# Optimization experiments

Hardware: AMD Instinct MI355X
Metric: run time of the kernel (lower is better)

Reference implementation:

```python
import jax, jax.numpy as jnp
import numpy as np

L = 2048
NODE_DIM = 64
EDGE_DIM = 32

def setup_inputs() -> dict:
    key = jax.random.key(0)
    ks = jax.random.split(key, 5)
    coords = jax.random.normal(ks[0], (L, 3), dtype=jnp.float32) * 10.0
    node_features = jax.random.normal(ks[1], (L, NODE_DIM), dtype=jnp.float32)
    pair_features = jax.random.normal(ks[2], (L, L, EDGE_DIM), dtype=jnp.float32)
    # haiku Linear params: w (in, out), b (out,)
    w_attn = jax.random.normal(ks[3], (EDGE_DIM + 1, 1), dtype=jnp.float32) / np.sqrt(EDGE_DIM + 1)
    b_attn = jnp.zeros((1,), dtype=jnp.float32)
    w_mag = jax.random.normal(ks[4], (NODE_DIM, 1), dtype=jnp.float32) / np.sqrt(NODE_DIM)
    b_mag = jnp.zeros((1,), dtype=jnp.float32)
    return {"coords": coords, "node_features": node_features, "pair_features": pair_features,
            "w_attn": w_attn, "b_attn": b_attn, "w_mag": w_mag, "b_mag": b_mag}

def reference(coords, node_features, pair_features, w_attn, b_attn, w_mag, b_mag):
    # displacements[i,j] = coords[i] - coords[j]  -> (L, L, 3)
    displacements = coords[:, None, :] - coords[None, :, :]
    distances = jnp.linalg.norm(displacements, axis=-1, keepdims=True) + 1e-08  # (L,L,1)
    directions = displacements / distances  # (L,L,3)
    # Linear(1) over concat(pair_features, distance): split the matvec to avoid concat copy
    # logits = [pair_features, dist] @ w_attn + b_attn  -> (L,L,1)
    attention_logits = (jnp.einsum('ije,eo->ijo', pair_features, w_attn[:-1])
                        + distances * w_attn[-1] + b_attn)
    attention_weights = jax.nn.softmax(attention_logits, axis=1)  # softmax over j-index axis 1
    update_magnitudes = jnp.tanh(node_features @ w_mag + b_mag) * 0.1  # (L,1)
    # sum over axis=1 of attn * dir * mag[:,None,:]
    coord_updates = jnp.sum(attention_weights * directions, axis=1) * update_magnitudes  # (L,3)
    return coords + coord_updates
```

## Files before the change

kernel.cpp:

```cpp
#include <hip/hip_runtime.h>
#include <math.h>

#define LL 2048
#define NODE_DIM 64
#define EDGE_DIM 32
#define LOG2E 1.4426950408889634f

typedef float vfloat4 __attribute__((ext_vector_type(4)));

__global__ __launch_bounds__(256, 6) void se3_layer_kernel(
    const float* __restrict__ coords,
    const float* __restrict__ node_features,
    const float* __restrict__ pair,
    const float* __restrict__ w_attn,
    const float* __restrict__ b_attn,
    const float* __restrict__ w_mag,
    const float* __restrict__ b_mag,
    float* __restrict__ out)
{
    __shared__ float s_cx[LL], s_cy[LL], s_cz[LL];
    __shared__ float s_mag;
    __shared__ float r_m[4], r_s[4], r_ax[4], r_ay[4], r_az[4];

    const int i    = blockIdx.x;
    const int tid  = threadIdx.x;
    const int lane = tid & 63;
    const int wave = tid >> 6;
    const int sub  = lane & 7;
    const int grp  = lane >> 3;

    for (int j = tid; j < LL; j += 256) {
        s_cx[j] = coords[3 * j + 0];
        s_cy[j] = coords[3 * j + 1];
        s_cz[j] = coords[3 * j + 2];
    }

    if (tid < NODE_DIM) {
        float v = node_features[(size_t)i * NODE_DIM + tid] * w_mag[tid];
        #pragma unroll
        for (int off = 32; off; off >>= 1) v += __shfl_xor(v, off);
        if (tid == 0) s_mag = tanhf(v + b_mag[0]) * 0.1f;
    }
    __syncthreads();

    const float w0 = w_attn[4 * sub + 0] * LOG2E;
    const float w1 = w_attn[4 * sub + 1] * LOG2E;
    const float w2 = w_attn[4 * sub + 2] * LOG2E;
    const float w3 = w_attn[4 * sub + 3] * LOG2E;
    const float wd = w_attn[EDGE_DIM] * LOG2E;
    const float bb = b_attn[0] * LOG2E;
    const float cix = s_cx[i], ciy = s_cy[i], ciz = s_cz[i];

    float m = -INFINITY, s = 0.f, ax = 0.f, ay = 0.f, az = 0.f;

    const vfloat4* prow = (const vfloat4*)(pair + (size_t)i * LL * EDGE_DIM);

    auto process = [&](vfloat4 v, int jbase) {
        float dotv = v.x * w0 + v.y * w1 + v.z * w2 + v.w * w3;
        dotv += __shfl_xor(dotv, 1);
        dotv += __shfl_xor(dotv, 2);
        dotv += __shfl_xor(dotv, 4);

        const int j = jbase + grp;
        float dx = cix - s_cx[j], dy = ciy - s_cy[j], dz = ciz - s_cz[j];
        float d2 = fmaf(dx, dx, fmaf(dy, dy, dz * dz));
        d2 = fmaxf(d2, 1e-24f);
        float r    = __builtin_amdgcn_rsqf(d2);
        float dist = d2 * r;
        float logit = fmaf(dist, wd, dotv + bb);

        float mn    = fmaxf(m, logit);
        float scale = __builtin_amdgcn_exp2f(m - mn);
        float pw    = __builtin_amdgcn_exp2f(logit - mn);
        s  = fmaf(s,  scale, pw);
        float px = pw * r;
        ax = fmaf(ax, scale, px * dx);
        ay = fmaf(ay, scale, px * dy);
        az = fmaf(az, scale, px * dz);
        m = mn;
    };

    int J = wave * 16;
    vfloat4 a0 = __builtin_nontemporal_load(&prow[(size_t)J * 8 + lane]);
    vfloat4 a1 = __builtin_nontemporal_load(&prow[(size_t)(J + 8) * 8 + lane]);
    for (int it = 1; it < 32; ++it) {
        const int Jn = it * 64 + wave * 16;
        vfloat4 b0 = __builtin_nontemporal_load(&prow[(size_t)Jn * 8 + lane]);
        vfloat4 b1 = __builtin_nontemporal_load(&prow[(size_t)(Jn + 8) * 8 + lane]);
        process(a0, J);
        process(a1, J + 8);
        a0 = b0; a1 = b1; J = Jn;
    }
    process(a0, J);
    process(a1, J + 8);

    #pragma unroll
    for (int off = 32; off; off >>= 1) {
        float m2  = __shfl_xor(m,  off);
        float s2  = __shfl_xor(s,  off);
        float ax2 = __shfl_xor(ax, off);
        float ay2 = __shfl_xor(ay, off);
        float az2 = __shfl_xor(az, off);
        float M  = fmaxf(m, m2);
        float c1 = __builtin_amdgcn_exp2f(m - M), c2 = __builtin_amdgcn_exp2f(m2 - M);
        s  = s  * c1 + s2  * c2;
        ax = ax * c1 + ax2 * c2;
        ay = ay * c1 + ay2 * c2;
        az = az * c1 + az2 * c2;
        m = M;
    }

    if (lane == 0) {
        r_m[wave] = m; r_s[wave] = s;
        r_ax[wave] = ax; r_ay[wave] = ay; r_az[wave] = az;
    }
    __syncthreads();

    if (tid == 0) {
        float M = r_m[0], S = r_s[0], AX = r_ax[0], AY = r_ay[0], AZ = r_az[0];
        #pragma unroll
        for (int w = 1; w < 4; ++w) {
            float M2 = r_m[w];
            float Mn = fmaxf(M, M2);
            float c1 = __builtin_amdgcn_exp2f(M - Mn), c2 = __builtin_amdgcn_exp2f(M2 - Mn);
            S  = S  * c1 + r_s[w]  * c2;
            AX = AX * c1 + r_ax[w] * c2;
            AY = AY * c1 + r_ay[w] * c2;
            AZ = AZ * c1 + r_az[w] * c2;
            M = Mn;
        }
        float inv_s = 1.0f / S;
        float mg = s_mag;
        out[3 * i + 0] = coords[3 * i + 0] + AX * inv_s * mg;
        out[3 * i + 1] = coords[3 * i + 1] + AY * inv_s * mg;
        out[3 * i + 2] = coords[3 * i + 2] + AZ * inv_s * mg;
    }
}

extern "C" void kernel_launch(void* const* d_in, const int* in_sizes, int n_in,
                              void* d_out, int out_size, void* d_ws, size_t ws_size,
                              hipStream_t stream) {
    const float* coords        = (const float*)d_in[0];
    const float* node_features = (const float*)d_in[1];
    const float* pair          = (const float*)d_in[2];
    const float* w_attn        = (const float*)d_in[3];
    const float* b_attn        = (const float*)d_in[4];
    const float* w_mag         = (const float*)d_in[5];
    const float* b_mag         = (const float*)d_in[6];
    float* out = (float*)d_out;

    se3_layer_kernel<<<LL, 256, 0, stream>>>(coords, node_features, pair,
                                             w_attn, b_attn, w_mag, b_mag, out);
}
```

Baseline: 92.58 us.

## Process two query rows per block to reuse coordinate tile and halve blocks

```diff
diff --git a/kernel.cpp b/kernel.cpp
--- a/kernel.cpp
+++ b/kernel.cpp
@@ -8,7 +8,7 @@
 
 typedef float vfloat4 __attribute__((ext_vector_type(4)));
 
-__global__ __launch_bounds__(256, 6) void se3_layer_kernel(
+__global__ __launch_bounds__(256, 4) void se3_layer_kernel(
     const float* __restrict__ coords,
     const float* __restrict__ node_features,
     const float* __restrict__ pair,
@@ -19,15 +19,23 @@
     float* __restrict__ out)
 {
     __shared__ float s_cx[LL], s_cy[LL], s_cz[LL];
-    __shared__ float s_mag;
-    __shared__ float r_m[4], r_s[4], r_ax[4], r_ay[4], r_az[4];
+    __shared__ float s_mag[2];
+    __shared__ float r_m[2][4], r_s[2][4], r_ax[2][4], r_ay[2][4], r_az[2][4];
 
-    const int i    = blockIdx.x;
+    const int i0   = 2 * blockIdx.x;
+    const int i1   = i0 + 1;
     const int tid  = threadIdx.x;
     const int lane = tid & 63;
     const int wave = tid >> 6;
     const int sub  = lane & 7;
     const int grp  = lane >> 3;
+
+    const vfloat4* prow0 = (const vfloat4*)(pair + (size_t)i0 * LL * EDGE_DIM);
+    const vfloat4* prow1 = (const vfloat4*)(pair + (size_t)i1 * LL * EDGE_DIM);
+
+    int J = wave * 8;
+    vfloat4 a0 = __builtin_nontemporal_load(&prow0[(size_t)J * 8 + lane]);
+    vfloat4 a1 = __builtin_nontemporal_load(&prow1[(size_t)J * 8 + lane]);
 
     for (int j = tid; j < LL; j += 256) {
         s_cx[j] = coords[3 * j + 0];
@@ -35,11 +43,11 @@
         s_cz[j] = coords[3 * j + 2];
     }
 
-    if (tid < NODE_DIM) {
-        float v = node_features[(size_t)i * NODE_DIM + tid] * w_mag[tid];
+    if (wave < 2) {
+        float v = node_features[(size_t)(i0 + wave) * NODE_DIM + lane] * w_mag[lane];
         #pragma unroll
         for (int off = 32; off; off >>= 1) v += __shfl_xor(v, off);
-        if (tid == 0) s_mag = tanhf(v + b_mag[0]) * 0.1f;
+        if (lane == 0) s_mag[wave] = tanhf(v + b_mag[0]) * 0.1f;
     }
     __syncthreads();
 
@@ -49,91 +57,113 @@
     const float w3 = w_attn[4 * sub + 3] * LOG2E;
     const float wd = w_attn[EDGE_DIM] * LOG2E;
     const float bb = b_attn[0] * LOG2E;
-    const float cix = s_cx[i], ciy = s_cy[i], ciz = s_cz[i];
+    const float c0x = s_cx[i0], c0y = s_cy[i0], c0z = s_cz[i0];
+    const float c1x = s_cx[i1], c1y = s_cy[i1], c1z = s_cz[i1];
 
-    float m = -INFINITY, s = 0.f, ax = 0.f, ay = 0.f, az = 0.f;
+    float m0 = -INFINITY, s0 = 0.f, ax0 = 0.f, ay0 = 0.f, az0 = 0.f;
+    float m1 = -INFINITY, s1 = 0.f, ax1 = 0.f, ay1 = 0.f, az1 = 0.f;
 
-    const vfloat4* prow = (const vfloat4*)(pair + (size_t)i * LL * EDGE_DIM);
-
-    auto process = [&](vfloat4 v, int jbase) {
-        float dotv = v.x * w0 + v.y * w1 + v.z * w2 + v.w * w3;
-        dotv += __shfl_xor(dotv, 1);
-        dotv += __shfl_xor(dotv, 2);
-        dotv += __shfl_xor(dotv, 4);
+    auto process = [&](vfloat4 v0, vfloat4 v1, int jbase) {
+        float d0 = v0.x * w0 + v0.y * w1 + v0.z * w2 + v0.w * w3;
+        float d1 = v1.x * w0 + v1.y * w1 + v1.z * w2 + v1.w * w3;
+        d0 += __shfl_xor(d0, 1);  d1 += __shfl_xor(d1, 1);
+        d0 += __shfl_xor(d0, 2);  d1 += __shfl_xor(d1, 2);
+        d0 += __shfl_xor(d0, 4);  d1 += __shfl_xor(d1, 4);
 
         const int j = jbase + grp;
-        float dx = cix - s_cx[j], dy = ciy - s_cy[j], dz = ciz - s_cz[j];
-        float d2 = fmaf(dx, dx, fmaf(dy, dy, dz * dz));
-        d2 = fmaxf(d2, 1e-24f);
-        float r    = __builtin_amdgcn_rsqf(d2);
-        float dist = d2 * r;
-        float logit = fmaf(dist, wd, dotv + bb);
+        const float cx = s_cx[j], cy = s_cy[j], cz = s_cz[j];
 
-        float mn    = fmaxf(m, logit);
-        float scale = __builtin_amdgcn_exp2f(m - mn);
-        float pw    = __builtin_amdgcn_exp2f(logit - mn);
-        s  = fmaf(s,  scale, pw);
-        float px = pw * r;
-        ax = fmaf(ax, scale, px * dx);
-        ay = fmaf(ay, scale, px * dy);
-        az = fmaf(az, scale, px * dz);
-        m = mn;
+        {
+            float dx = c0x - cx, dy = c0y - cy, dz = c0z - cz;
+            float d2 = fmaf(dx, dx, fmaf(dy, dy, dz * dz));
+            d2 = fmaxf(d2, 1e-24f);
+            float r    = __builtin_amdgcn_rsqf(d2);
+            float dist = d2 * r;
+            float logit = fmaf(dist, wd, d0 + bb);
+            float mn    = fmaxf(m0, logit);
+            float scale = __builtin_amdgcn_exp2f(m0 - mn);
+            float pw    = __builtin_amdgcn_exp2f(logit - mn);
+            s0  = fmaf(s0,  scale, pw);
+            float px = pw * r;
+            ax0 = fmaf(ax0, scale, px * dx);
+            ay0 = fmaf(ay0, scale, px * dy);
+            az0 = fmaf(az0, scale, px * dz);
+            m0 = mn;
+        }
+        {
+            float dx = c1x - cx, dy = c1y - cy, dz = c1z - cz;
+            float d2 = fmaf(dx, dx, fmaf(dy, dy, dz * dz));
+            d2 = fmaxf(d2, 1e-24f);
+            float r    = __builtin_amdgcn_rsqf(d2);
+            float dist = d2 * r;
+            float logit = fmaf(dist, wd, d1 + bb);
+            float mn    = fmaxf(m1, logit);
+            float scale = __builtin_amdgcn_exp2f(m1 - mn);
+            float pw    = __builtin_amdgcn_exp2f(logit - mn);
+            s1  = fmaf(s1,  scale, pw);
+            float px = pw * r;
+            ax1 = fmaf(ax1, scale, px * dx);
+            ay1 = fmaf(ay1, scale, px * dy);
+            az1 = fmaf(az1, scale, px * dz);
+            m1 = mn;
+        }
     };
 
-    int J = wave * 16;
-    vfloat4 a0 = __builtin_nontemporal_load(&prow[(size_t)J * 8 + lane]);
-    vfloat4 a1 = __builtin_nontemporal_load(&prow[(size_t)(J + 8) * 8 + lane]);
-    for (int it = 1; it < 32; ++it) {
-        const int Jn = it * 64 + wave * 16;
-        vfloat4 b0 = __builtin_nontemporal_load(&prow[(size_t)Jn * 8 + lane]);
-        vfloat4 b1 = __builtin_nontemporal_load(&prow[(size_t)(Jn + 8) * 8 + lane]);
-        process(a0, J);
-        process(a1, J + 8);
+    for (int it = 1; it < 64; ++it) {
+        const int Jn = it * 32 + wave * 8;
+        vfloat4 b0 = __builtin_nontemporal_load(&prow0[(size_t)Jn * 8 + lane]);
+        vfloat4 b1 = __builtin_nontemporal_load(&prow1[(size_t)Jn * 8 + lane]);
+        process(a0, a1, J);
         a0 = b0; a1 = b1; J = Jn;
     }
-    process(a0, J);
-    process(a1, J + 8);
+    process(a0, a1, J);
 
     #pragma unroll
     for (int off = 32; off; off >>= 1) {
-        float m2  = __shfl_xor(m,  off);
-        float s2  = __shfl_xor(s,  off);
-        float ax2 = __shfl_xor(ax, off);
-        float ay2 = __shfl_xor(ay, off);
-        float az2 = __shfl_xor(az, off);
-        float M  = fmaxf(m, m2);
-        float c1 = __builtin_amdgcn_exp2f(m - M), c2 = __builtin_amdgcn_exp2f(m2 - M);
-        s  = s  * c1 + s2  * c2;
-        ax = ax * c1 + ax2 * c2;
-        ay = ay * c1 + ay2 * c2;
-        az = az * c1 + az2 * c2;
-        m = M;
+        float m2, sx, bx, by, bz, M, e1, e2;
+        m2 = __shfl_xor(m0, off); sx = __shfl_xor(s0, off);
+        bx = __shfl_xor(ax0, off); by = __shfl_xor(ay0, off); bz = __shfl_xor(az0, off);
+        M = fmaxf(m0, m2);
+        e1 = __builtin_amdgcn_exp2f(m0 - M); e2 = __builtin_amdgcn_exp2f(m2 - M);
+        s0 = s0 * e1 + sx * e2; ax0 = ax0 * e1 + bx * e2;
+        ay0 = ay0 * e1 + by * e2; az0 = az0 * e1 + bz * e2; m0 = M;
+
+        m2 = __shfl_xor(m1, off); sx = __shfl_xor(s1, off);
+        bx = __shfl_xor(ax1, off); by = __shfl_xor(ay1, off); bz = __shfl_xor(az1, off);
+        M = fmaxf(m1, m2);
+        e1 = __builtin_amdgcn_exp2f(m1 - M); e2 = __builtin_amdgcn_exp2f(m2 - M);
+        s1 = s1 * e1 + sx * e2; ax1 = ax1 * e1 + bx * e2;
+        ay1 = ay1 * e1 + by * e2; az1 = az1 * e1 + bz * e2; m1 = M;
     }
 
     if (lane == 0) {
-        r_m[wave] = m; r_s[wave] = s;
-        r_ax[wave] = ax; r_ay[wave] = ay; r_az[wave] = az;
+        r_m[0][wave] = m0; r_s[0][wave] = s0;
+        r_ax[0][wave] = ax0; r_ay[0][wave] = ay0; r_az[0][wave] = az0;
+        r_m[1][wave] = m1; r_s[1][wave] = s1;
+        r_ax[1][wave] = ax1; r_ay[1][wave] = ay1; r_az[1][wave] = az1;
     }
     __syncthreads();
 
-    if (tid == 0) {
-        float M = r_m[0], S = r_s[0], AX = r_ax[0], AY = r_ay[0], AZ = r_az[0];
+    if (wave == 0 && lane < 2) {
+        const int row = lane;
+        const int i = i0 + row;
+        float M = r_m[row][0], S = r_s[row][0];
+        float AX = r_ax[row][0], AY = r_ay[row][0], AZ = r_az[row][0];
         #pragma unroll
         for (int w = 1; w < 4; ++w) {
-            float M2 = r_m[w];
+            float M2 = r_m[row][w];
             float Mn = fmaxf(M, M2);
-            float c1 = __builtin_amdgcn_exp2f(M - Mn), c2 = __builtin_amdgcn_exp2f(M2 - Mn);
-            S  = S  * c1 + r_s[w]  * c2;
-            AX = AX * c1 + r_ax[w] * c2;
-            AY = AY * c1 + r_ay[w] * c2;
-            AZ = AZ * c1 + r_az[w] * c2;
+            float e1 = __builtin_amdgcn_exp2f(M - Mn), e2 = __builtin_amdgcn_exp2f(M2 - Mn);
+            S  = S  * e1 + r_s[row][w]  * e2;
+            AX = AX * e1 + r_ax[row][w] * e2;
+            AY = AY * e1 + r_ay[row][w] * e2;
+            AZ = AZ * e1 + r_az[row][w] * e2;
             M = Mn;
         }
-        float inv_s = 1.0f / S;
-        float mg = s_mag;
-        out[3 * i + 0] = coords[3 * i + 0] + AX * inv_s * mg;
-        out[3 * i + 1] = coords[3 * i + 1] + AY * inv_s * mg;
-        out[3 * i + 2] = coords[3 * i + 2] + AZ * inv_s * mg;
+        float k = s_mag[row] / S;
+        out[3 * i + 0] = coords[3 * i + 0] + AX * k;
+        out[3 * i + 1] = coords[3 * i + 1] + AY * k;
+        out[3 * i + 2] = coords[3 * i + 2] + AZ * k;
     }
 }
 
@@ -149,6 +179,6 @@
     const float* b_mag         = (const float*)d_in[6];
     float* out = (float*)d_out;
 
-    se3_layer_kernel<<<LL, 256, 0, stream>>>(coords, node_features, pair,
-                                             w_attn, b_attn, w_mag, b_mag, out);
+    se3_layer_kernel<<<LL / 2, 256, 0, stream>>>(coords, node_features, pair,
+                                                 w_attn, b_attn, w_mag, b_mag, out);
 }
```

Result: no change. 91.54 us (-1.1%).
